# Kernel tuning notes

Hardware: AMD Instinct MI355X
Metric: run time of the kernel (lower is better)

The kernel has to match this reference:

```python
import jax, jax.numpy as jnp
import numpy as np

N_NODES = 100000
N_EDGES = 6400000
IN_CH = 128
NEG_SLOPE = 0.2


def setup_inputs() -> dict:
    key = jax.random.key(0)
    k1, k2, k3, k4, k5 = jax.random.split(key, 5)
    x = jax.random.normal(k1, (N_NODES, IN_CH), dtype=jnp.float32)
    edge_index = jax.random.randint(k2, (2, N_EDGES), 0, N_NODES, dtype=jnp.int64)
    # GATConv params (heads=1, out_channels=1): glorot-style scale
    W = jax.random.normal(k3, (IN_CH, 1), dtype=jnp.float32) / np.sqrt(IN_CH)
    att_src = jax.random.normal(k4, (1,), dtype=jnp.float32)
    att_dst = jax.random.normal(k5, (1,), dtype=jnp.float32)
    bias = jnp.zeros((1,), dtype=jnp.float32)
    return {"x": x, "edge_index": edge_index, "W": W,
            "att_src": att_src, "att_dst": att_dst, "bias": bias}


def reference(x, edge_index, W, att_src, att_dst, bias):
    N = x.shape[0]
    h = (x @ W)[:, 0]                      # [N] projected features (out_channels=1)
    # add self-loops (PyG default add_self_loops=True)
    loop = jnp.arange(N, dtype=edge_index.dtype)
    src = jnp.concatenate([edge_index[0], loop])   # [E+N]
    dst = jnp.concatenate([edge_index[1], loop])
    a_s = h * att_src[0]                   # per-node src attention term
    a_d = h * att_dst[0]                   # per-node dst attention term
    logits = jax.nn.leaky_relu(a_s[src] + a_d[dst], NEG_SLOPE)  # [E+N]
    # segment softmax over incoming edges of each destination node
    seg_max = jax.ops.segment_max(logits, dst, num_segments=N)
    e = jnp.exp(logits - seg_max[dst])
    denom = jax.ops.segment_sum(e, dst, num_segments=N)
    alpha = e / (denom[dst] + 1e-16)
    # scatter-aggregate weighted source features
    out = jax.ops.segment_sum(alpha * h[src], dst, num_segments=N)  # [N]
    return out[:, None] + bias             # [N, 1]
```

## Files before the change

### kernel.cpp

```cpp
#include <hip/hip_runtime.h>

#define IN_CH 128
#define NEG_SLOPE 0.2f
#define BINSZ 8000
#define NBINS 13
#define NW 8192
#define MAX_SG 39
#define MAX_BPB 40
#define F_NUM 2097152.0f
#define F_DEN 16777216.0f
#define INV_F_NUM 4.76837158203125e-7f
#define INV_F_DEN 5.9604644775390625e-8f

typedef int   vi4 __attribute__((ext_vector_type(4)));
typedef float vf4 __attribute__((ext_vector_type(4)));

__device__ __forceinline__ float lrelu(float v) { return v > 0.f ? v : NEG_SLOPE * v; }
__device__ __forceinline__ unsigned enc_max(float f) {
    unsigned u = __float_as_uint(f);
    return (u & 0x80000000u) ? ~u : (u | 0x80000000u);
}
__device__ __forceinline__ float dec_max(unsigned e) {
    return (e & 0x80000000u) ? __uint_as_float(e ^ 0x80000000u) : __uint_as_float(~e);
}

__device__ __forceinline__ void do_proj(const float* __restrict__ x, const float* __restrict__ W,
                                        const float* __restrict__ att_dst,
                                        float* __restrict__ h, float* __restrict__ ad_h,
                                        int n, int wid, int nwaves) {
    int lane = threadIdx.x & 63;
    int half = lane >> 5;
    int hl   = lane & 31;

    vf4 w4 = reinterpret_cast<const vf4*>(W)[hl];
    const float ad = att_dst[0];

    int npair = n >> 1;
    for (int p0 = wid * 4; p0 < npair; p0 += nwaves * 4) {
        float s[4];
        #pragma unroll
        for (int k = 0; k < 4; ++k) {
            int p = p0 + k;
            s[k] = 0.f;
            if (p < npair) {
                int row = 2 * p + half;
                vf4 v = __builtin_nontemporal_load(
                    reinterpret_cast<const vf4*>(x + (size_t)row * IN_CH) + hl);
                s[k] = v.x * w4.x + v.y * w4.y + v.z * w4.z + v.w * w4.w;
            }
        }
        #pragma unroll
        for (int k = 0; k < 4; ++k) {
            #pragma unroll
            for (int off = 16; off > 0; off >>= 1) s[k] += __shfl_xor(s[k], off);
        }
        #pragma unroll
        for (int k = 0; k < 4; ++k) {
            int p = p0 + k;
            if (p < npair && hl == 0) {
                int row = 2 * p + half;
                h[row] = s[k];
                ad_h[row] = s[k] * ad;
            }
        }
    }
    if ((n & 1) && wid == 0) {
        int row = n - 1;
        vf4 v = reinterpret_cast<const vf4*>(x + (size_t)row * IN_CH)[hl];
        float s = v.x * w4.x + v.y * w4.y + v.z * w4.z + v.w * w4.w;
        #pragma unroll
        for (int off = 16; off > 0; off >>= 1) s += __shfl_xor(s, off);
        if (lane == 0) { h[row] = s; ad_h[row] = s * ad; }
    }
}

__global__ __launch_bounds__(256)
void proj_kernel(const float* __restrict__ x, const float* __restrict__ W,
                 const float* __restrict__ att_dst,
                 float* __restrict__ h, float* __restrict__ ad_h, int n) {
    int wid    = (blockIdx.x * blockDim.x + threadIdx.x) >> 6;
    int nwaves = (gridDim.x * blockDim.x) >> 6;
    do_proj(x, W, att_dst, h, ad_h, n, wid, nwaves);
}

__global__ __launch_bounds__(256)
void hmax_kernel(const float* __restrict__ h,
                 const float* __restrict__ att_src, const float* __restrict__ att_dst,
                 unsigned* __restrict__ maxenc, int n) {
    const float as = att_src[0];
    const float ad = att_dst[0];
    float m1 = -1e30f, m2 = -1e30f;
    for (int i = blockIdx.x * blockDim.x + threadIdx.x; i < n;
         i += gridDim.x * blockDim.x) {
        float v = h[i];
        m1 = fmaxf(m1, v * as);
        m2 = fmaxf(m2, v * ad);
    }
    #pragma unroll
    for (int off = 32; off > 0; off >>= 1) {
        m1 = fmaxf(m1, __shfl_xor(m1, off));
        m2 = fmaxf(m2, __shfl_xor(m2, off));
    }
    __shared__ float bm[2][4];
    int wv = threadIdx.x >> 6;
    if ((threadIdx.x & 63) == 0) { bm[0][wv] = m1; bm[1][wv] = m2; }
    __syncthreads();
    if (threadIdx.x == 0) {
        float a = fmaxf(fmaxf(bm[0][0], bm[0][1]), fmaxf(bm[0][2], bm[0][3]));
        float b = fmaxf(fmaxf(bm[1][0], bm[1][1]), fmaxf(bm[1][2], bm[1][3]));
        atomicMax(maxenc,     enc_max(a));
        atomicMax(maxenc + 1, enc_max(b));
    }
}

__global__ __launch_bounds__(256)
void count_kernel(const int* __restrict__ dst_idx, int* __restrict__ wc, int E) {
    int lane = threadIdx.x & 63, wv = threadIdx.x >> 6;
    int g = blockIdx.x * 4 + wv;
    long long E4 = E >> 2;
    long long e0 = 4 * (E4 * g / NW);
    long long e1 = (g == NW - 1) ? (long long)E : 4 * (E4 * (g + 1) / NW);

    int cnt = 0;
    for (long long i0 = e0; i0 < e1; i0 += 64) {
        long long i = i0 + lane;
        int b = NBINS;
        if (i < e1) b = __builtin_nontemporal_load(dst_idx + i) / BINSZ;
        #pragma unroll
        for (int b2 = 0; b2 < NBINS; ++b2) {
            unsigned long long m = __ballot(b == b2);
            if (lane == b2) cnt += __popcll(m);
        }
    }
    if (lane < NBINS) wc[lane * NW + g] = cnt;
}

__global__ __launch_bounds__(256)
void scanA_kernel(const int* __restrict__ wc, int* __restrict__ bsum) {
    __shared__ int wt[4];
    int t = threadIdx.x, lane = t & 63, wv = t >> 6;
    vi4 c = *reinterpret_cast<const vi4*>(wc + blockIdx.x * 1024 + 4 * t);
    int s = c.x + c.y + c.z + c.w;
    #pragma unroll
    for (int off = 32; off > 0; off >>= 1) s += __shfl_xor(s, off);
    if (lane == 0) wt[wv] = s;
    __syncthreads();
    if (t == 0) bsum[blockIdx.x] = wt[0] + wt[1] + wt[2] + wt[3];
}

__global__ __launch_bounds__(128)
void scanB_kernel(const int* __restrict__ bsum, int* __restrict__ bbase,
                  int* __restrict__ rbase, int* __restrict__ hist, int nchunk) {
    __shared__ int sb[129];
    __shared__ int wt[2];
    int t = threadIdx.x, lane = t & 63, wv = t >> 6;
    int v = (t < nchunk) ? bsum[t] : 0;
    int inc = v;
    #pragma unroll
    for (int d2 = 1; d2 < 64; d2 <<= 1) { int u = __shfl_up(inc, d2); if (lane >= d2) inc += u; }
    if (lane == 63) wt[wv] = inc;
    __syncthreads();
    int excl = ((wv == 1) ? wt[0] : 0) + inc - v;
    sb[t] = excl;
    if (t == 127) sb[128] = excl + v;
    __syncthreads();
    if (t < nchunk) bbase[t] = sb[t];
    if (t < NBINS) {
        int rb = sb[t * (NW / 1024)];
        rbase[t] = rb;
        int nb = (t == NBINS - 1) ? sb[128] : sb[(t + 1) * (NW / 1024)];
        hist[t] = nb - rb;
    }
}

__global__ __launch_bounds__(256)
void scanC_kernel(const int* __restrict__ wc, const int* __restrict__ bbase,
                  int* __restrict__ wbase) {
    __shared__ int wt[4];
    int t = threadIdx.x, lane = t & 63, wv = t >> 6;
    int base = blockIdx.x * 1024 + 4 * t;
    vi4 c = *reinterpret_cast<const vi4*>(wc + base);
    int s0 = c.x, s1 = s0 + c.y, s2 = s1 + c.z, s3 = s2 + c.w;
    int tot = s3;
    int inc = tot;
    #pragma unroll
    for (int d2 = 1; d2 < 64; d2 <<= 1) { int u = __shfl_up(inc, d2); if (lane >= d2) inc += u; }
    if (lane == 63) wt[wv] = inc;
    __syncthreads();
    int wb = 0;
    for (int k = 0; k < wv; ++k) wb += wt[k];
    int excl = bbase[blockIdx.x] + wb + inc - tot;
    vi4 o; o.x = excl; o.y = excl + s0; o.z = excl + s1; o.w = excl + s2;
    *reinterpret_cast<vi4*>(wbase + base) = o;
}

__global__ __launch_bounds__(256)
void place_proj_kernel(const int* __restrict__ src_idx, const int* __restrict__ dst_idx,
                       const int* __restrict__ wbase, unsigned* __restrict__ rec, int E,
                       const float* __restrict__ x, const float* __restrict__ W,
                       const float* __restrict__ att_dst,
                       float* __restrict__ h, float* __restrict__ ad_h, int n) {
    int b = blockIdx.x;
    int role = b % 3;
    if (role == 2) {
        int qid = b / 3;
        int wid = qid * 4 + (threadIdx.x >> 6);
        do_proj(x, W, att_dst, h, ad_h, n, wid, 4096);
        return;
    }
    int pid  = (b / 3) * 2 + role;
    int lane = threadIdx.x & 63, wv = threadIdx.x >> 6;
    int g = pid * 4 + wv;
    long long E4 = E >> 2;
    long long e0 = 4 * (E4 * g / NW);
    long long e1 = (g == NW - 1) ? (long long)E : 4 * (E4 * (g + 1) / NW);

    unsigned long long ltmask = (1ULL << lane) - 1;
    int cur = (lane < NBINS) ? wbase[lane * NW + g] : 0;

    for (long long i0 = e0; i0 < e1; i0 += 64) {
        long long i = i0 + lane;
        bool valid = (i < e1);
        int d = valid ? __builtin_nontemporal_load(dst_idx + i) : 0;
        int s = valid ? __builtin_nontemporal_load(src_idx + i) : 0;
        int bb = valid ? d / BINSZ : NBINS;
        int r  = d - (d / BINSZ) * BINSZ;
        int pos = 0;
        #pragma unroll
        for (int b2 = 0; b2 < NBINS; ++b2) {
            unsigned long long m = __ballot(bb == b2);
            int base_b = __shfl(cur, b2);
            if (bb == b2) pos = base_b + __popcll(m & ltmask);
            if (lane == b2) cur += __popcll(m);
        }
        if (valid) rec[pos] = ((unsigned)r << 17) | (unsigned)s;
    }
}

__global__ __launch_bounds__(1024)
void gather_kernel(const unsigned* __restrict__ rec,
                   const float* __restrict__ h, const float* __restrict__ ad_h,
                   const float* __restrict__ att_src, const unsigned* __restrict__ maxenc,
                   const int* __restrict__ rbase, const int* __restrict__ hist,
                   unsigned long long* __restrict__ part, int SG) {
    __shared__ __align__(16) unsigned long long s_acc[BINSZ];

    int bin   = blockIdx.x / SG;
    int slice = blockIdx.x - bin * SG;
    long long r0 = rbase[bin];
    int cnt   = hist[bin];
    long long g0 = r0 + (long long)cnt * slice / SG;
    long long g1 = r0 + (long long)cnt * (slice + 1) / SG;

    {
        vi4 z = {0, 0, 0, 0};
        for (int k = threadIdx.x; k < BINSZ / 2; k += 1024)
            *reinterpret_cast<vi4*>(&s_acc[2 * k]) = z;
    }
    __syncthreads();

    const float as = att_src[0];
    const float L  = lrelu(dec_max(maxenc[0]) + dec_max(maxenc[1]));
    const float* adw = ad_h + bin * BINSZ;

    auto process1 = [&](unsigned q) {
        int s0 = q & 0x1FFFFu, ri = q >> 17;
        float h0 = h[s0];
        float e0 = __expf(lrelu(fmaf(h0, as, adw[ri])) - L);
        unsigned long long p0 = ((unsigned long long)(long long)__float2int_rn(e0 * h0 * F_NUM) << 32)
                              + __float2uint_rn(e0 * F_DEN);
        atomicAdd(&s_acc[ri], p0);
    };

    long long a0 = (g0 + 3) & ~3LL;
    long long a1 = g1 & ~3LL;
    long long headEnd, tail0;
    if (a0 <= a1) { headEnd = a0; tail0 = a1; }
    else          { headEnd = g1; tail0 = g1; a0 = 0; a1 = 0; }

    for (long long i = g0 + threadIdx.x; i < headEnd; i += 1024) process1(rec[i]);

    const long long step = 4096;
    long long iA = a0 + 4 * (long long)threadIdx.x;
    bool vA = (iA < a1);
    vi4 qA = {0,0,0,0};
    if (vA) qA = __builtin_nontemporal_load(reinterpret_cast<const vi4*>(rec + iA));

    long long iB = iA + step;
    bool vB = (iB < a1);
    vi4 qB = {0,0,0,0};
    if (vB) qB = __builtin_nontemporal_load(reinterpret_cast<const vi4*>(rec + iB));

    int   rA0=0, rA1=0, rA2=0, rA3=0;
    float hA0=0, hA1=0, hA2=0, hA3=0, dA0=0, dA1=0, dA2=0, dA3=0;
    if (vA) {
        unsigned u0=(unsigned)qA.x, u1=(unsigned)qA.y, u2=(unsigned)qA.z, u3=(unsigned)qA.w;
        int sA0=u0&0x1FFFFu, sA1=u1&0x1FFFFu, sA2=u2&0x1FFFFu, sA3=u3&0x1FFFFu;
        rA0=u0>>17; rA1=u1>>17; rA2=u2>>17; rA3=u3>>17;
        hA0=h[sA0]; hA1=h[sA1]; hA2=h[sA2]; hA3=h[sA3];
        dA0=adw[rA0]; dA1=adw[rA1]; dA2=adw[rA2]; dA3=adw[rA3];
    }

    while (vA) {
        long long iC = iB + step;
        bool vC = (iC < a1);
        vi4 qC = {0,0,0,0};
        if (vC) qC = __builtin_nontemporal_load(reinterpret_cast<const vi4*>(rec + iC));

        int   rB0=0, rB1=0, rB2=0, rB3=0;
        float hB0=0, hB1=0, hB2=0, hB3=0, dB0=0, dB1=0, dB2=0, dB3=0;
        if (vB) {
            unsigned u0=(unsigned)qB.x, u1=(unsigned)qB.y, u2=(unsigned)qB.z, u3=(unsigned)qB.w;
            int sB0=u0&0x1FFFFu, sB1=u1&0x1FFFFu, sB2=u2&0x1FFFFu, sB3=u3&0x1FFFFu;
            rB0=u0>>17; rB1=u1>>17; rB2=u2>>17; rB3=u3>>17;
            hB0=h[sB0]; hB1=h[sB1]; hB2=h[sB2]; hB3=h[sB3];
            dB0=adw[rB0]; dB1=adw[rB1]; dB2=adw[rB2]; dB3=adw[rB3];
        }

        float e0 = __expf(lrelu(fmaf(hA0, as, dA0)) - L);
        float e1 = __expf(lrelu(fmaf(hA1, as, dA1)) - L);
        float e2 = __expf(lrelu(fmaf(hA2, as, dA2)) - L);
        float e3 = __expf(lrelu(fmaf(hA3, as, dA3)) - L);
        unsigned long long p0 = ((unsigned long long)(long long)__float2int_rn(e0 * hA0 * F_NUM) << 32) + __float2uint_rn(e0 * F_DEN);
        unsigned long long p1 = ((unsigned long long)(long long)__float2int_rn(e1 * hA1 * F_NUM) << 32) + __float2uint_rn(e1 * F_DEN);
        unsigned long long p2 = ((unsigned long long)(long long)__float2int_rn(e2 * hA2 * F_NUM) << 32) + __float2uint_rn(e2 * F_DEN);
        unsigned long long p3 = ((unsigned long long)(long long)__float2int_rn(e3 * hA3 * F_NUM) << 32) + __float2uint_rn(e3 * F_DEN);
        atomicAdd(&s_acc[rA0], p0);
        atomicAdd(&s_acc[rA1], p1);
        atomicAdd(&s_acc[rA2], p2);
        atomicAdd(&s_acc[rA3], p3);

        vA = vB;
        rA0=rB0; rA1=rB1; rA2=rB2; rA3=rB3;
        hA0=hB0; hA1=hB1; hA2=hB2; hA3=hB3;
        dA0=dB0; dA1=dB1; dA2=dB2; dA3=dB3;
        vB = vC; qB = qC; iB = iC;
    }

    for (long long i2 = tail0 + threadIdx.x; i2 < g1; i2 += 1024) process1(rec[i2]);
    __syncthreads();

    unsigned long long* outp = part + (size_t)blockIdx.x * BINSZ;
    for (int k = threadIdx.x; k < BINSZ / 2; k += 1024) {
        vi4 v = *reinterpret_cast<const vi4*>(&s_acc[2 * k]);
        __builtin_nontemporal_store(v, reinterpret_cast<vi4*>(outp + 2 * k));
    }
}

__global__ void reduce_final(const unsigned long long* __restrict__ part,
                             const float* __restrict__ h,
                             const float* __restrict__ att_src, const float* __restrict__ att_dst,
                             const float* __restrict__ bias, const unsigned* __restrict__ maxenc,
                             float* __restrict__ out, int n, int SG) {
    int i = blockIdx.x * blockDim.x + threadIdx.x;
    if (i >= n) return;
    int bin = i / BINSZ;
    int off = i - bin * BINSZ;
    float num = 0.f, den = 0.f;
    const unsigned long long* p = part + (size_t)(bin * SG) * BINSZ;
    for (int s = 0; s < SG; ++s) {
        unsigned long long v = __builtin_nontemporal_load(p + off);
        num += (float)(int)(v >> 32);
        den += (float)(unsigned)(v & 0xffffffffULL);
        p += BINSZ;
    }
    num *= INV_F_NUM;
    den *= INV_F_DEN;
    const float L = lrelu(dec_max(maxenc[0]) + dec_max(maxenc[1]));
    float hv = h[i];
    float e  = __expf(lrelu(hv * (att_src[0] + att_dst[0])) - L);
    out[i] = (num + e * hv) / (den + e + 1e-30f) + bias[0];
}

__global__ __launch_bounds__(1024)
void binpass_kernel(const int* __restrict__ src_idx, const int* __restrict__ dst_idx,
                    const float* __restrict__ h,
                    const float* __restrict__ att_src, const float* __restrict__ att_dst,
                    float* __restrict__ part, int E, int n, int BPB) {
    __shared__ float s_num[BINSZ];
    __shared__ float s_den[BINSZ];

    int bin   = blockIdx.x / BPB;
    int slice = blockIdx.x - bin * BPB;
    int base  = bin * BINSZ;
    int blen  = min(BINSZ, n - base);

    for (int k = threadIdx.x; k < BINSZ; k += 1024) { s_num[k] = 0.f; s_den[k] = 0.f; }
    __syncthreads();

    const float as = att_src[0];
    const float ad = att_dst[0];

    long long e0 = (long long)E * slice / BPB;
    long long e1 = (long long)E * (slice + 1) / BPB;
    for (long long i = e0 + threadIdx.x; i < e1; i += 1024) {
        int d = dst_idx[i];
        unsigned r = (unsigned)(d - base);
        if (r < (unsigned)blen) {
            int s = src_idx[i];
            float hs = h[s];
            float v  = fmaf(hs, as, h[d] * ad);
            float e  = __expf(lrelu(v));
            atomicAdd(&s_num[r], e * hs);
            atomicAdd(&s_den[r], e);
        }
    }
    __syncthreads();

    float* outp = part + (size_t)blockIdx.x * (2 * BINSZ);
    for (int k = threadIdx.x; k < BINSZ; k += 1024) {
        outp[k]         = s_num[k];
        outp[BINSZ + k] = s_den[k];
    }
}

__global__ void fb_reduce_final(const float* __restrict__ part, const float* __restrict__ h,
                                const float* __restrict__ att_src, const float* __restrict__ att_dst,
                                const float* __restrict__ bias, float* __restrict__ out,
                                int n, int BPB) {
    int i = blockIdx.x * blockDim.x + threadIdx.x;
    if (i >= n) return;
    int bin = i / BINSZ;
    int off = i - bin * BINSZ;
    float num = 0.f, den = 0.f;
    const float* p = part + (size_t)(bin * BPB) * (2 * BINSZ);
    for (int s = 0; s < BPB; ++s) {
        num += p[off];
        den += p[BINSZ + off];
        p += 2 * BINSZ;
    }
    float hv = h[i];
    float e  = __expf(lrelu(hv * (att_src[0] + att_dst[0])));
    out[i] = (num + e * hv) / (den + e + 1e-16f) + bias[0];
}

__global__ void edge_kernel(const int* __restrict__ src_idx, const int* __restrict__ dst_idx,
                            const float* __restrict__ h,
                            const float* __restrict__ att_src, const float* __restrict__ att_dst,
                            float* __restrict__ nd, int E) {
    const float as = att_src[0];
    const float ad = att_dst[0];
    int i      = blockIdx.x * blockDim.x + threadIdx.x;
    int stride = gridDim.x * blockDim.x;
    for (; i < E; i += stride) {
        int s = src_idx[i];
        int d = dst_idx[i];
        float hs = h[s];
        float e  = __expf(lrelu(fmaf(hs, as, h[d] * ad)));
        unsafeAtomicAdd(&nd[2 * d],     e * hs);
        unsafeAtomicAdd(&nd[2 * d + 1], e);
    }
}

__global__ void final_kernel(const float* __restrict__ h, const float* __restrict__ nd,
                             const float* __restrict__ att_src, const float* __restrict__ att_dst,
                             const float* __restrict__ bias, float* __restrict__ out, int n) {
    int i = blockIdx.x * blockDim.x + threadIdx.x;
    if (i >= n) return;
    float hv = h[i];
    float e  = __expf(lrelu(hv * (att_src[0] + att_dst[0])));
    out[i] = (nd[2 * i] + e * hv) / (nd[2 * i + 1] + e + 1e-16f) + bias[0];
}

extern "C" void kernel_launch(void* const* d_in, const int* in_sizes, int n_in,
                              void* d_out, int out_size, void* d_ws, size_t ws_size,
                              hipStream_t stream) {
    const float* x       = (const float*)d_in[0];
    const int*   ei      = (const int*)d_in[1];
    const float* W       = (const float*)d_in[2];
    const float* att_src = (const float*)d_in[3];
    const float* att_dst = (const float*)d_in[4];
    const float* bias    = (const float*)d_in[5];
    float*       out     = (float*)d_out;

    const int n = out_size;
    const int E = in_sizes[1] / 2;

    const int NELEM  = NBINS * NW;
    const int NCHUNK = NELEM / 1024;

    size_t off = 0;
    auto alloc = [&](size_t bytes) { size_t p = off; off = (off + bytes + 255) & ~(size_t)255; return p; };
    size_t o_h    = alloc((size_t)n * sizeof(float));
    size_t o_adh  = alloc((size_t)n * sizeof(float));
    size_t o_wc   = alloc((size_t)NELEM * sizeof(int));
    size_t o_wb   = alloc((size_t)NELEM * sizeof(int));
    size_t o_bs   = alloc((size_t)NCHUNK * sizeof(int));
    size_t o_bb   = alloc((size_t)NCHUNK * sizeof(int));
    size_t o_meta = alloc(64 * sizeof(int));
    size_t o_rec  = alloc((size_t)E * sizeof(unsigned));
    size_t fixed  = off;

    float*    h      = (float*)((char*)d_ws + o_h);
    float*    ad_h   = (float*)((char*)d_ws + o_adh);
    int*      rbase  = (int*)((char*)d_ws + o_meta);
    int*      hist   = rbase + 16;
    unsigned* maxenc = (unsigned*)(rbase + 32);
    const size_t per = (size_t)BINSZ * sizeof(unsigned long long);

    int SG = 0;
    if (ws_size > fixed) SG = (int)((ws_size - fixed) / ((size_t)NBINS * per));
    if (SG > MAX_SG) SG = MAX_SG;

    bool ok_shape = (n <= NBINS * BINSZ) && ((E & 3) == 0) && (E >= 4 * NW) && ((n & 1) == 0);

    if (SG >= 8 && ok_shape) {
        int*                wc   = (int*)((char*)d_ws + o_wc);
        int*                wb   = (int*)((char*)d_ws + o_wb);
        int*                bsum = (int*)((char*)d_ws + o_bs);
        int*                bbase= (int*)((char*)d_ws + o_bb);
        unsigned*           rec  = (unsigned*)((char*)d_ws + o_rec);
        unsigned long long* part = (unsigned long long*)((char*)d_ws + fixed);

        hipMemsetAsync(maxenc, 0, 2 * sizeof(unsigned), stream);
        count_kernel<<<NW / 4, 256, 0, stream>>>(ei + E, wc, E);
        scanA_kernel<<<NCHUNK, 256, 0, stream>>>(wc, bsum);
        scanB_kernel<<<1, 128, 0, stream>>>(bsum, bbase, rbase, hist, NCHUNK);
        scanC_kernel<<<NCHUNK, 256, 0, stream>>>(wc, bbase, wb);
        place_proj_kernel<<<3072, 256, 0, stream>>>(ei, ei + E, wb, rec, E,
                                                    x, W, att_dst, h, ad_h, n);
        hmax_kernel<<<120, 256, 0, stream>>>(h, att_src, att_dst, maxenc, n);
        gather_kernel<<<NBINS * SG, 1024, 0, stream>>>(rec, h, ad_h, att_src, maxenc,
                                                       rbase, hist, part, SG);
        reduce_final<<<(n + 255) / 256, 256, 0, stream>>>(part, h, att_src, att_dst,
                                                          bias, maxenc, out, n, SG);
    } else {
        proj_kernel<<<1024, 256, 0, stream>>>(x, W, att_dst, h, ad_h, n);
        size_t hb = (((size_t)n * 2 * sizeof(float)) + 255) & ~(size_t)255;
        int BPB = 0;
        if (ws_size > hb) BPB = (int)((ws_size - hb) / ((size_t)NBINS * per));
        if (BPB > MAX_BPB) BPB = MAX_BPB;

        if (BPB >= 6 && n <= NBINS * BINSZ) {
            float* part = (float*)((char*)d_ws + hb);
            binpass_kernel<<<NBINS * BPB, 1024, 0, stream>>>(
                ei, ei + E, h, att_src, att_dst, part, E, n, BPB);
            fb_reduce_final<<<(n + 255) / 256, 256, 0, stream>>>(
                part, h, att_src, att_dst, bias, out, n, BPB);
        } else {
            float* nd = (float*)((char*)d_ws + hb);
            hipMemsetAsync(nd, 0, (size_t)n * 2 * sizeof(float), stream);
            edge_kernel<<<2048, 256, 0, stream>>>(ei, ei + E, h, att_src, att_dst, nd, E);
            final_kernel<<<(n + 255) / 256, 256, 0, stream>>>(h, nd, att_src, att_dst,
                                                              bias, out, n);
        }
    }
}
```

Baseline: 144.5 us.

## Move projection into count pass and use LDS-atomic vectorized placement

The node projection now runs as extra blocks of the count kernel instead of the placement kernel. The placement kernel loads four edges per lane with vector loads and takes bin slots with shared-memory atomicAdd on per-wave cursors, replacing the per-bin ballot/shuffle loop. This cuts ALU and cross-lane work in placement. Edge order within a bin is no longer deterministic, and LDS atomic contention on popular bins could serialize.

```diff
diff --git a/kernel.cpp b/kernel.cpp
--- a/kernel.cpp
+++ b/kernel.cpp
@@ -84,6 +84,40 @@
 }
 
 __global__ __launch_bounds__(256)
+void count_proj_kernel(const int* __restrict__ dst_idx, int* __restrict__ wc, int E,
+                       const float* __restrict__ x, const float* __restrict__ W,
+                       const float* __restrict__ att_dst,
+                       float* __restrict__ h, float* __restrict__ ad_h, int n) {
+    int b = blockIdx.x;
+    int role = b % 3;
+    if (role == 2) {
+        int qid = b / 3;
+        int wid = qid * 4 + (threadIdx.x >> 6);
+        do_proj(x, W, att_dst, h, ad_h, n, wid, 4096);
+        return;
+    }
+    int pid  = (b / 3) * 2 + role;
+    int lane = threadIdx.x & 63, wv = threadIdx.x >> 6;
+    int g = pid * 4 + wv;
+    long long E4 = E >> 2;
+    long long e0 = 4 * (E4 * g / NW);
+    long long e1 = (g == NW - 1) ? (long long)E : 4 * (E4 * (g + 1) / NW);
+
+    int cnt = 0;
+    for (long long i0 = e0; i0 < e1; i0 += 64) {
+        long long i = i0 + lane;
+        int bb = NBINS;
+        if (i < e1) bb = __builtin_nontemporal_load(dst_idx + i) / BINSZ;
+        #pragma unroll
+        for (int b2 = 0; b2 < NBINS; ++b2) {
+            unsigned long long m = __ballot(bb == b2);
+            if (lane == b2) cnt += __popcll(m);
+        }
+    }
+    if (lane < NBINS) wc[lane * NW + g] = cnt;
+}
+
+__global__ __launch_bounds__(256)
 void hmax_kernel(const float* __restrict__ h,
                  const float* __restrict__ att_src, const float* __restrict__ att_dst,
                  unsigned* __restrict__ maxenc, int n) {
@@ -111,28 +145,6 @@
         atomicMax(maxenc,     enc_max(a));
         atomicMax(maxenc + 1, enc_max(b));
     }
-}
-
-__global__ __launch_bounds__(256)
-void count_kernel(const int* __restrict__ dst_idx, int* __restrict__ wc, int E) {
-    int lane = threadIdx.x & 63, wv = threadIdx.x >> 6;
-    int g = blockIdx.x * 4 + wv;
-    long long E4 = E >> 2;
-    long long e0 = 4 * (E4 * g / NW);
-    long long e1 = (g == NW - 1) ? (long long)E : 4 * (E4 * (g + 1) / NW);
-
-    int cnt = 0;
-    for (long long i0 = e0; i0 < e1; i0 += 64) {
-        long long i = i0 + lane;
-        int b = NBINS;
-        if (i < e1) b = __builtin_nontemporal_load(dst_idx + i) / BINSZ;
-        #pragma unroll
-        for (int b2 = 0; b2 < NBINS; ++b2) {
-            unsigned long long m = __ballot(b == b2);
-            if (lane == b2) cnt += __popcll(m);
-        }
-    }
-    if (lane < NBINS) wc[lane * NW + g] = cnt;
 }
 
 __global__ __launch_bounds__(256)
@@ -195,45 +207,32 @@
 }
 
 __global__ __launch_bounds__(256)
-void place_proj_kernel(const int* __restrict__ src_idx, const int* __restrict__ dst_idx,
-                       const int* __restrict__ wbase, unsigned* __restrict__ rec, int E,
-                       const float* __restrict__ x, const float* __restrict__ W,
-                       const float* __restrict__ att_dst,
-                       float* __restrict__ h, float* __restrict__ ad_h, int n) {
-    int b = blockIdx.x;
-    int role = b % 3;
-    if (role == 2) {
-        int qid = b / 3;
-        int wid = qid * 4 + (threadIdx.x >> 6);
-        do_proj(x, W, att_dst, h, ad_h, n, wid, 4096);
-        return;
-    }
-    int pid  = (b / 3) * 2 + role;
+void place_kernel(const int* __restrict__ src_idx, const int* __restrict__ dst_idx,
+                  const int* __restrict__ wbase, unsigned* __restrict__ rec, int E) {
+    __shared__ int ccur[4][NBINS];
     int lane = threadIdx.x & 63, wv = threadIdx.x >> 6;
-    int g = pid * 4 + wv;
+    int g = blockIdx.x * 4 + wv;
+    if (lane < NBINS) ccur[wv][lane] = wbase[lane * NW + g];
+    __syncthreads();
+
     long long E4 = E >> 2;
     long long e0 = 4 * (E4 * g / NW);
     long long e1 = (g == NW - 1) ? (long long)E : 4 * (E4 * (g + 1) / NW);
-
-    unsigned long long ltmask = (1ULL << lane) - 1;
-    int cur = (lane < NBINS) ? wbase[lane * NW + g] : 0;
-
-    for (long long i0 = e0; i0 < e1; i0 += 64) {
-        long long i = i0 + lane;
-        bool valid = (i < e1);
-        int d = valid ? __builtin_nontemporal_load(dst_idx + i) : 0;
-        int s = valid ? __builtin_nontemporal_load(src_idx + i) : 0;
-        int bb = valid ? d / BINSZ : NBINS;
-        int r  = d - (d / BINSZ) * BINSZ;
-        int pos = 0;
-        #pragma unroll
-        for (int b2 = 0; b2 < NBINS; ++b2) {
-            unsigned long long m = __ballot(bb == b2);
-            int base_b = __shfl(cur, b2);
-            if (bb == b2) pos = base_b + __popcll(m & ltmask);
-            if (lane == b2) cur += __popcll(m);
-        }
-        if (valid) rec[pos] = ((unsigned)r << 17) | (unsigned)s;
+    for (long long i0 = e0; i0 < e1; i0 += 256) {
+        long long i = i0 + 4 * lane;
+        if (i < e1) {
+            vi4 d4 = __builtin_nontemporal_load(reinterpret_cast<const vi4*>(dst_idx + i));
+            vi4 s4 = __builtin_nontemporal_load(reinterpret_cast<const vi4*>(src_idx + i));
+            int b0 = d4.x / BINSZ, b1 = d4.y / BINSZ, b2 = d4.z / BINSZ, b3 = d4.w / BINSZ;
+            int p0 = atomicAdd(&ccur[wv][b0], 1);
+            int p1 = atomicAdd(&ccur[wv][b1], 1);
+            int p2 = atomicAdd(&ccur[wv][b2], 1);
+            int p3 = atomicAdd(&ccur[wv][b3], 1);
+            rec[p0] = ((unsigned)(d4.x - b0 * BINSZ) << 17) | (unsigned)s4.x;
+            rec[p1] = ((unsigned)(d4.y - b1 * BINSZ) << 17) | (unsigned)s4.y;
+            rec[p2] = ((unsigned)(d4.z - b2 * BINSZ) << 17) | (unsigned)s4.z;
+            rec[p3] = ((unsigned)(d4.w - b3 * BINSZ) << 17) | (unsigned)s4.w;
+        }
     }
 }
 
@@ -513,12 +512,12 @@
         unsigned long long* part = (unsigned long long*)((char*)d_ws + fixed);
 
         hipMemsetAsync(maxenc, 0, 2 * sizeof(unsigned), stream);
-        count_kernel<<<NW / 4, 256, 0, stream>>>(ei + E, wc, E);
+        count_proj_kernel<<<3072, 256, 0, stream>>>(ei + E, wc, E,
+                                                    x, W, att_dst, h, ad_h, n);
         scanA_kernel<<<NCHUNK, 256, 0, stream>>>(wc, bsum);
         scanB_kernel<<<1, 128, 0, stream>>>(bsum, bbase, rbase, hist, NCHUNK);
         scanC_kernel<<<NCHUNK, 256, 0, stream>>>(wc, bbase, wb);
-        place_proj_kernel<<<3072, 256, 0, stream>>>(ei, ei + E, wb, rec, E,
-                                                    x, W, att_dst, h, ad_h, n);
+        place_kernel<<<NW / 4, 256, 0, stream>>>(ei, ei + E, wb, rec, E);
         hmax_kernel<<<120, 256, 0, stream>>>(h, att_src, att_dst, maxenc, n);
         gather_kernel<<<NBINS * SG, 1024, 0, stream>>>(rec, h, ad_h, att_src, maxenc,
                                                        rbase, hist, part, SG);
```

Measured after the change: 134.3 us. 7.1% less time.
